# Optimization experiments

Measured on AMD Instinct MI355X. Metric: run time of the kernel, lower is better.

The kernel has to match this reference:

```python
import jax, jax.numpy as jnp
import numpy as np

ALPHA = 0.2  # LeakyReLU negative slope
NEG_INF = -9e15


def setup_inputs() -> dict:
    key = jax.random.key(0)
    k1, k2, k3, k4 = jax.random.split(key, 4)
    B, N, Fin, Fout = 4, 4096, 128, 64
    x = jax.random.normal(k1, (B, N, Fin), dtype=jnp.float32)
    adj = jax.random.randint(k2, (B, N, N), 0, 2, dtype=jnp.int32)
    # xavier_uniform-ish init scale
    W = jax.random.normal(k3, (Fin, Fout), dtype=jnp.float32) * (1.414 / np.sqrt(Fin + Fout))
    a = jax.random.normal(k4, (3 * Fout, 1), dtype=jnp.float32) * (1.414 / np.sqrt(3 * Fout + 1))
    return {"x": x, "adj": adj, "W": W, "a": a}


def reference(x, adj, W, a):
    # h: [B, N, Fout]
    h = jnp.matmul(x, W)
    Fout = W.shape[1]
    # Original builds a_input[b,i,j] = [h_i, h_j, h_i*h_j] and dots with a.
    # Decompose a into the three blocks; identical math, no O(N^2*3F) tensor.
    a1 = a[:Fout, 0]            # weights on h_i (self)
    a2 = a[Fout:2 * Fout, 0]    # weights on h_j (neighbor)
    a3 = a[2 * Fout:, 0]        # weights on h_i * h_j (corr)
    s_self = jnp.einsum('bnf,f->bn', h, a1)        # [B,N]
    s_nei = jnp.einsum('bnf,f->bn', h, a2)         # [B,N]
    s_corr = jnp.einsum('bif,bjf->bij', h * a3, h)  # [B,N,N]
    e = s_self[:, :, None] + s_nei[:, None, :] + s_corr
    e = jnp.where(e > 0, e, ALPHA * e)  # LeakyReLU
    att = jnp.where(adj > 0, e, NEG_INF)
    att = jax.nn.softmax(att, axis=-1)
    # dropout=0.0 / eval mode -> no dropout
    h_prime = jnp.matmul(att, h)  # [B,N,Fout]
    return jax.nn.elu(h_prime)    # concat=True
```

## Files before the change

kernel.cpp:

```cpp
#include <hip/hip_runtime.h>


typedef __attribute__((ext_vector_type(4))) float f32x4;
typedef __attribute__((ext_vector_type(4))) _Float16 h16x4;
typedef __attribute__((ext_vector_type(8))) _Float16 h16x8;
typedef __attribute__((ext_vector_type(2))) __fp16 fp16x2;

#define L2E 1.4426950408889634f

__global__ __launch_bounds__(256) void gat_phase1(
    const float* __restrict__ x,
    const float* __restrict__ W,
    const float* __restrict__ a,
    _Float16* __restrict__ h16,
    _Float16* __restrict__ hT16,
    _Float16* __restrict__ q16,
    float* __restrict__ sS,
    float* __restrict__ sN)
{
  __shared__ float xs[32 * 132];
  __shared__ float ws[128 * 64];
  const int tid = threadIdx.x;
  const int bx  = blockIdx.x;
  const int b   = bx >> 7;
  const int n0  = (bx & 127) << 5;
  const float* xb = x + ((size_t)b * 4096 + n0) * 128;

#pragma unroll
  for (int p = 0; p < 4; ++p) {
    int idx = tid + p * 256;
    int row = idx >> 5, c4 = idx & 31;
    float4 v = ((const float4*)(xb + row * 128))[c4];
    *(float4*)&xs[row * 132 + c4 * 4] = v;
  }
#pragma unroll
  for (int p = 0; p < 8; ++p) {
    int idx = tid + p * 256;
    ((float4*)ws)[idx] = ((const float4*)W)[idx];
  }
  __syncthreads();

  const int tx = tid & 15;
  const int ty = tid >> 4;
  f32x4 acc0 = (f32x4){0.f, 0.f, 0.f, 0.f};
  f32x4 acc1 = (f32x4){0.f, 0.f, 0.f, 0.f};

#pragma unroll 8
  for (int k = 0; k < 128; k += 4) {
    f32x4 x0 = *(const f32x4*)&xs[(2 * ty) * 132 + k];
    f32x4 x1 = *(const f32x4*)&xs[(2 * ty + 1) * 132 + k];
    f32x4 w0 = *(const f32x4*)&ws[(k + 0) * 64 + 4 * tx];
    f32x4 w1 = *(const f32x4*)&ws[(k + 1) * 64 + 4 * tx];
    f32x4 w2 = *(const f32x4*)&ws[(k + 2) * 64 + 4 * tx];
    f32x4 w3 = *(const f32x4*)&ws[(k + 3) * 64 + 4 * tx];
    acc0 += x0.x * w0 + x0.y * w1 + x0.z * w2 + x0.w * w3;
    acc1 += x1.x * w0 + x1.y * w1 + x1.z * w2 + x1.w * w3;
  }
  float acc[2][4] = {{acc0.x, acc0.y, acc0.z, acc0.w},
                     {acc1.x, acc1.y, acc1.z, acc1.w}};

  float a1r[4], a2r[4], a3r[4];
#pragma unroll
  for (int f = 0; f < 4; ++f) {
    a1r[f] = a[4 * tx + f] * L2E;
    a2r[f] = a[64 + 4 * tx + f] * L2E;
    a3r[f] = a[128 + 4 * tx + f] * L2E;
  }
  const size_t bN = (size_t)b * 4096;
#pragma unroll
  for (int r = 0; r < 2; ++r) {
    float p1 = 0.f, p2 = 0.f;
#pragma unroll
    for (int f = 0; f < 4; ++f) { p1 += acc[r][f] * a1r[f]; p2 += acc[r][f] * a2r[f]; }
#pragma unroll
    for (int m = 1; m < 16; m <<= 1) {
      p1 += __shfl_xor(p1, m, 64);
      p2 += __shfl_xor(p2, m, 64);
    }
    if (tx == 0) {
      int n = n0 + 2 * ty + r;
      sS[bN + n] = p1;
      sN[bN + n] = p2;
    }
  }
#pragma unroll
  for (int r = 0; r < 2; ++r) {
    int n = n0 + 2 * ty + r;
    h16x4 hv, qv;
#pragma unroll
    for (int f = 0; f < 4; ++f) {
      hv[f] = (_Float16)acc[r][f];
      qv[f] = (_Float16)(acc[r][f] * a3r[f]);
    }
    *(h16x4*)&h16[(bN + n) * 64 + 4 * tx] = hv;
    *(h16x4*)&q16[(bN + n) * 64 + 4 * tx] = qv;
  }
  __syncthreads();
  _Float16* hTs = (_Float16*)xs;
#pragma unroll
  for (int f = 0; f < 4; ++f)
#pragma unroll
    for (int r = 0; r < 2; ++r)
      hTs[(4 * tx + f) * 40 + 2 * ty + r] = (_Float16)acc[r][f];
  __syncthreads();
  {
    int f = tid >> 2, part = tid & 3;
    uint4 v = *(uint4*)&hTs[f * 40 + 8 * part];
    *(uint4*)&hT16[((size_t)b * 64 + f) * 4096 + n0 + 8 * part] = v;
  }
}

__global__ __launch_bounds__(256, 4) void gat_phase2(
    const _Float16* __restrict__ h16,
    const _Float16* __restrict__ hT16,
    const _Float16* __restrict__ q16,
    const float* __restrict__ sS,
    const float* __restrict__ sN,
    const int* __restrict__ adj,
    float* __restrict__ Opart,
    float* __restrict__ lpart)
{
  __shared__ _Float16 Kb[2][4096];
  __shared__ _Float16 Tb[2][4096];
  __shared__ float sNl[1024];

  const int tid = threadIdx.x;
  const int w = tid >> 6, lane = tid & 63;
  const int qd = lane >> 4, c = lane & 15;
  const int bx = blockIdx.x;
  const int b = bx & 3;
  const int split = (bx >> 2) & 3;
  const int it = bx >> 4;
  const int i0 = it * 64 + w * 16;
  const int jq0 = split * 1024;
  const size_t bN = (size_t)b * 4096;

  const _Float16* qrow = q16 + (bN + i0 + c) * 64;
  h16x8 Qf0 = *(const h16x8*)(qrow + qd * 8);
  h16x8 Qf1 = *(const h16x8*)(qrow + 32 + qd * 8);
  const float ss = sS[bN + i0 + c];

  const int* abase = adj + (bN + i0 + c) * 4096 + jq0 + 4 * qd;

  const int srow = tid >> 3, chunk = tid & 7;
  const int ksw = (chunk ^ (srow & 7)) << 3;
  const int tsw = (chunk ^ ((srow >> 1) & 7)) << 3;
  const bool tswap = (srow & 1);
  const _Float16* hsrc = h16 + (bN + jq0 + srow) * 64 + chunk * 8;
  const _Float16* tsrc = hT16 + ((size_t)b * 64 + srow) * 4096 + jq0 + chunk * 8;

  f32x4 O[4];
#pragma unroll
  for (int ft = 0; ft < 4; ++ft) O[ft] = (f32x4){0.f, 0.f, 0.f, 0.f};
  float lsum = 0.f;

  {
    uint4 k0 = *(const uint4*)hsrc, k1 = *(const uint4*)(hsrc + 32 * 64);
    uint4 t0 = *(const uint4*)tsrc, t1 = *(const uint4*)(tsrc + 32 * 4096);
    *(uint4*)&Kb[0][srow * 64 + ksw] = k0;
    *(uint4*)&Kb[0][(srow + 32) * 64 + ksw] = k1;
    uint4 s0 = tswap ? (uint4){t0.z, t0.w, t0.x, t0.y} : t0;
    uint4 s1 = tswap ? (uint4){t1.z, t1.w, t1.x, t1.y} : t1;
    *(uint4*)&Tb[0][srow * 64 + tsw] = s0;
    *(uint4*)&Tb[0][(srow + 32) * 64 + tsw] = s1;
  }
  ((f32x4*)sNl)[tid] = *(const f32x4*)(sN + bN + jq0 + 4 * tid);
  uint4 av[4];
#pragma unroll
  for (int ct = 0; ct < 4; ++ct) av[ct] = *(const uint4*)(abase + 16 * ct);

  for (int t = 0; t < 16; ++t) {
    __syncthreads();

    uint4 kr0, kr1, tr0, tr1;
    uint4 avn[4] = {av[0], av[1], av[2], av[3]};
    if (t < 15) {
      const _Float16* hs = hsrc + (t + 1) * 4096;
      const _Float16* ts = tsrc + (t + 1) * 64;
      kr0 = *(const uint4*)hs; kr1 = *(const uint4*)(hs + 32 * 64);
      tr0 = *(const uint4*)ts; tr1 = *(const uint4*)(ts + 32 * 4096);
#pragma unroll
      for (int ct = 0; ct < 4; ++ct)
        avn[ct] = *(const uint4*)(abase + (t + 1) * 64 + 16 * ct);
    }

    const _Float16* Kc = &Kb[t & 1][0];
    const _Float16* Tc = &Tb[t & 1][0];
#pragma unroll
    for (int ct = 0; ct < 4; ++ct) {
      const int krow = 16 * ct + c;
      h16x8 Kf0 = *(const h16x8*)&Kc[krow * 64 + ((qd ^ (c & 7)) << 3)];
      h16x8 Kf1 = *(const h16x8*)&Kc[krow * 64 + (((qd + 4) ^ (c & 7)) << 3)];
      f32x4 Sv = (f32x4){0.f, 0.f, 0.f, 0.f};
      Sv = __builtin_amdgcn_mfma_f32_16x16x32_f16(Kf0, Qf0, Sv, 0, 0, 0);
      Sv = __builtin_amdgcn_mfma_f32_16x16x32_f16(Kf1, Qf1, Sv, 0, 0, 0);

      f32x4 snv = ((const f32x4*)sNl)[t * 16 + 4 * ct + qd];
      f32x4 ev = Sv + snv + ss;
      f32x4 tv = __builtin_elementwise_max(ev, ev * 0.2f);
      float p0 = __builtin_amdgcn_exp2f(tv.x);
      float p1 = __builtin_amdgcn_exp2f(tv.y);
      float p2 = __builtin_amdgcn_exp2f(tv.z);
      float p3 = __builtin_amdgcn_exp2f(tv.w);
      p0 = av[ct].x ? p0 : 0.f;
      p1 = av[ct].y ? p1 : 0.f;
      p2 = av[ct].z ? p2 : 0.f;
      p3 = av[ct].w ? p3 : 0.f;
      lsum += (p0 + p1) + (p2 + p3);
      fp16x2 plo = __builtin_amdgcn_cvt_pkrtz(p0, p1);
      fp16x2 phi = __builtin_amdgcn_cvt_pkrtz(p2, p3);
      h16x4 Pf = (h16x4){(_Float16)plo.x, (_Float16)plo.y,
                         (_Float16)phi.x, (_Float16)phi.y};

#pragma unroll
      for (int ft = 0; ft < 4; ++ft) {
        h16x4 Vf = *(const h16x4*)&Tc[(16 * ft + c) * 64 +
                                      (((4 * ct + qd) ^ c) << 2)];
        O[ft] = __builtin_amdgcn_mfma_f32_16x16x16f16(Vf, Pf, O[ft], 0, 0, 0);
      }
    }

    if (t < 15) {
      _Float16* K2 = &Kb[(t & 1) ^ 1][0];
      _Float16* T2 = &Tb[(t & 1) ^ 1][0];
      *(uint4*)&K2[srow * 64 + ksw] = kr0;
      *(uint4*)&K2[(srow + 32) * 64 + ksw] = kr1;
      uint4 s0 = tswap ? (uint4){tr0.z, tr0.w, tr0.x, tr0.y} : tr0;
      uint4 s1 = tswap ? (uint4){tr1.z, tr1.w, tr1.x, tr1.y} : tr1;
      *(uint4*)&T2[srow * 64 + tsw] = s0;
      *(uint4*)&T2[(srow + 32) * 64 + tsw] = s1;
    }
#pragma unroll
    for (int ct = 0; ct < 4; ++ct) av[ct] = avn[ct];
  }

  lsum += __shfl_xor(lsum, 16, 64);
  lsum += __shfl_xor(lsum, 32, 64);

  float* orow = Opart + ((size_t)split * 16384 + bN + i0 + c) * 64;
#pragma unroll
  for (int ft = 0; ft < 4; ++ft)
    *(f32x4*)(orow + 16 * ft + 4 * qd) = O[ft];
  if (lane < 16) lpart[split * 16384 + bN + i0 + c] = lsum;
}

__global__ __launch_bounds__(256) void gat_combine(
    const float* __restrict__ Opart, const float* __restrict__ lpart,
    float* __restrict__ out)
{
  const int tid = threadIdx.x;
  const size_t row = (size_t)blockIdx.x * 16 + (tid >> 4);
  const int f4 = (tid & 15) * 4;
  const size_t R = 16384;
  float l = lpart[row] + lpart[R + row] + lpart[2 * R + row] + lpart[3 * R + row];
  f32x4 o = *(const f32x4*)&Opart[row * 64 + f4];
  o += *(const f32x4*)&Opart[(R + row) * 64 + f4];
  o += *(const f32x4*)&Opart[(2 * R + row) * 64 + f4];
  o += *(const f32x4*)&Opart[(3 * R + row) * 64 + f4];
  float inv = 1.0f / l;
  float4 res;
  float v;
  v = o.x * inv; res.x = v > 0.f ? v : __expf(v) - 1.f;
  v = o.y * inv; res.y = v > 0.f ? v : __expf(v) - 1.f;
  v = o.z * inv; res.z = v > 0.f ? v : __expf(v) - 1.f;
  v = o.w * inv; res.w = v > 0.f ? v : __expf(v) - 1.f;
  *(float4*)&out[row * 64 + f4] = res;
}

extern "C" void kernel_launch(void* const* d_in, const int* in_sizes, int n_in,
                              void* d_out, int out_size, void* d_ws, size_t ws_size,
                              hipStream_t stream) {
  const float* x  = (const float*)d_in[0];
  const int* adj  = (const int*)d_in[1];
  const float* W  = (const float*)d_in[2];
  const float* a  = (const float*)d_in[3];
  float* out = (float*)d_out;

  char* ws = (char*)d_ws;
  _Float16* h16  = (_Float16*)(ws);
  _Float16* hT16 = (_Float16*)(ws + (2u << 20));
  _Float16* q16  = (_Float16*)(ws + (4u << 20));
  float* sS = (float*)(ws + (6u << 20));
  float* sN = (float*)(ws + (6u << 20) + (64u << 10));
  float* Opart = (float*)(ws + (6u << 20) + (128u << 10));
  float* lpart = (float*)(ws + (6u << 20) + (128u << 10) + (17u << 20));

  gat_phase1<<<512, 256, 0, stream>>>(x, W, a, h16, hT16, q16, sS, sN);
  gat_phase2<<<1024, 256, 0, stream>>>(h16, hT16, q16, sS, sN, adj, Opart, lpart);
  gat_combine<<<1024, 256, 0, stream>>>(Opart, lpart, out);
}
```

Measured before the change: 394.5 us.

## Precompute adjacency bitmask in separate kernel and consume bits in attention pass

Adds a pre-pass kernel that streams the int32 adjacency matrix and packs it into 64-bit ballot bitmasks. The attention kernel then reads one 64-bit word per 64 columns instead of sixteen int32 values per lane per tile. This cuts that kernel's memory traffic and register use for adjacency prefetch, so its loop can be bound by compute rather than memory. In exchange there is an extra launch and a full pass over adjacency with narrow 4-byte loads, so the large read is moved rather than removed.

```diff
diff --git a/kernel.cpp b/kernel.cpp
--- a/kernel.cpp
+++ b/kernel.cpp
@@ -7,6 +7,23 @@
 typedef __attribute__((ext_vector_type(2))) __fp16 fp16x2;
 
 #define L2E 1.4426950408889634f
+
+__global__ __launch_bounds__(256) void gat_mask(
+    const int* __restrict__ adj,
+    unsigned long long* __restrict__ mask)
+{
+  const int tid = threadIdx.x;
+  const int w = tid >> 6, lane = tid & 63;
+  const size_t row = (size_t)blockIdx.x * 4 + w;
+  const int* ap = adj + row * 4096 + lane;
+  unsigned long long* mp = mask + row * 64;
+#pragma unroll 4
+  for (int s = 0; s < 64; ++s) {
+    int v = ap[s * 64];
+    unsigned long long m = __ballot(v > 0);
+    if (lane == 0) mp[s] = m;
+  }
+}
 
 __global__ __launch_bounds__(256) void gat_phase1(
     const float* __restrict__ x,
@@ -116,7 +133,7 @@
     const _Float16* __restrict__ q16,
     const float* __restrict__ sS,
     const float* __restrict__ sN,
-    const int* __restrict__ adj,
+    const unsigned long long* __restrict__ mask,
     float* __restrict__ Opart,
     float* __restrict__ lpart)
 {
@@ -140,7 +157,7 @@
   h16x8 Qf1 = *(const h16x8*)(qrow + 32 + qd * 8);
   const float ss = sS[bN + i0 + c];
 
-  const int* abase = adj + (bN + i0 + c) * 4096 + jq0 + 4 * qd;
+  const unsigned long long* mrow = mask + (bN + i0 + c) * 64 + (jq0 >> 6);
 
   const int srow = tid >> 3, chunk = tid & 7;
   const int ksw = (chunk ^ (srow & 7)) << 3;
@@ -165,23 +182,19 @@
     *(uint4*)&Tb[0][(srow + 32) * 64 + tsw] = s1;
   }
   ((f32x4*)sNl)[tid] = *(const f32x4*)(sN + bN + jq0 + 4 * tid);
-  uint4 av[4];
-#pragma unroll
-  for (int ct = 0; ct < 4; ++ct) av[ct] = *(const uint4*)(abase + 16 * ct);
+  unsigned long long m64 = mrow[0];
 
   for (int t = 0; t < 16; ++t) {
     __syncthreads();
 
     uint4 kr0, kr1, tr0, tr1;
-    uint4 avn[4] = {av[0], av[1], av[2], av[3]};
+    unsigned long long mn = m64;
     if (t < 15) {
       const _Float16* hs = hsrc + (t + 1) * 4096;
       const _Float16* ts = tsrc + (t + 1) * 64;
       kr0 = *(const uint4*)hs; kr1 = *(const uint4*)(hs + 32 * 64);
       tr0 = *(const uint4*)ts; tr1 = *(const uint4*)(ts + 32 * 4096);
-#pragma unroll
-      for (int ct = 0; ct < 4; ++ct)
-        avn[ct] = *(const uint4*)(abase + (t + 1) * 64 + 16 * ct);
+      mn = mrow[t + 1];
     }
 
     const _Float16* Kc = &Kb[t & 1][0];
@@ -198,14 +211,15 @@
       f32x4 snv = ((const f32x4*)sNl)[t * 16 + 4 * ct + qd];
       f32x4 ev = Sv + snv + ss;
       f32x4 tv = __builtin_elementwise_max(ev, ev * 0.2f);
+      unsigned bits = (unsigned)(m64 >> (16 * ct + 4 * qd));
       float p0 = __builtin_amdgcn_exp2f(tv.x);
       float p1 = __builtin_amdgcn_exp2f(tv.y);
       float p2 = __builtin_amdgcn_exp2f(tv.z);
       float p3 = __builtin_amdgcn_exp2f(tv.w);
-      p0 = av[ct].x ? p0 : 0.f;
-      p1 = av[ct].y ? p1 : 0.f;
-      p2 = av[ct].z ? p2 : 0.f;
-      p3 = av[ct].w ? p3 : 0.f;
+      p0 = (bits & 1u) ? p0 : 0.f;
+      p1 = (bits & 2u) ? p1 : 0.f;
+      p2 = (bits & 4u) ? p2 : 0.f;
+      p3 = (bits & 8u) ? p3 : 0.f;
       lsum += (p0 + p1) + (p2 + p3);
       fp16x2 plo = __builtin_amdgcn_cvt_pkrtz(p0, p1);
       fp16x2 phi = __builtin_amdgcn_cvt_pkrtz(p2, p3);
@@ -230,8 +244,7 @@
       *(uint4*)&T2[srow * 64 + tsw] = s0;
       *(uint4*)&T2[(srow + 32) * 64 + tsw] = s1;
     }
-#pragma unroll
-    for (int ct = 0; ct < 4; ++ct) av[ct] = avn[ct];
+    m64 = mn;
   }
 
   lsum += __shfl_xor(lsum, 16, 64);
@@ -284,8 +297,11 @@
   float* sN = (float*)(ws + (6u << 20) + (64u << 10));
   float* Opart = (float*)(ws + (6u << 20) + (128u << 10));
   float* lpart = (float*)(ws + (6u << 20) + (128u << 10) + (17u << 20));
-
+  unsigned long long* mask =
+      (unsigned long long*)(ws + (6u << 20) + (128u << 10) + (18u << 20));
+
+  gat_mask<<<4096, 256, 0, stream>>>(adj, mask);
   gat_phase1<<<512, 256, 0, stream>>>(x, W, a, h16, hT16, q16, sS, sN);
-  gat_phase2<<<1024, 256, 0, stream>>>(h16, hT16, q16, sS, sN, adj, Opart, lpart);
+  gat_phase2<<<1024, 256, 0, stream>>>(h16, hT16, q16, sS, sN, mask, Opart, lpart);
   gat_combine<<<1024, 256, 0, stream>>>(Opart, lpart, out);
 }
```

Result: slower. 440.0 us (+11.5%).

## Precompute adjacency bitmask in separate kernel and consume bits in attention loop

Applied to the files above, without the earlier changes.

Adds a kernel that converts the int32 adjacency matrix into a 64-bit-per-word bitmask using wave ballots. The main attention kernel then loads 8-byte mask words instead of streaming 16-byte int vectors per step. This cuts adjacency traffic and register pressure inside the compute loop, at the cost of an extra launch and a separate full pass over adj.

```diff
diff --git a/kernel.cpp b/kernel.cpp
--- a/kernel.cpp
+++ b/kernel.cpp
@@ -5,8 +5,35 @@
 typedef __attribute__((ext_vector_type(4))) _Float16 h16x4;
 typedef __attribute__((ext_vector_type(8))) _Float16 h16x8;
 typedef __attribute__((ext_vector_type(2))) __fp16 fp16x2;
+typedef unsigned long long u64;
 
 #define L2E 1.4426950408889634f
+
+__global__ __launch_bounds__(256) void gat_mask(
+    const int* __restrict__ adj,
+    u64* __restrict__ mask)
+{
+  const int tid = threadIdx.x;
+  const int w = tid >> 6, lane = tid & 63;
+  const size_t row = blockIdx.x;
+  const int* ap = adj + row * 4096;
+  u64* mp = mask + row * 64;
+#pragma unroll
+  for (int p = 0; p < 4; ++p) {
+    const int k = w + 4 * p;
+    int4 v = *(const int4*)(ap + k * 256 + 4 * lane);
+    u64 b0 = __ballot(v.x > 0);
+    u64 b1 = __ballot(v.y > 0);
+    u64 b2 = __ballot(v.z > 0);
+    u64 b3 = __ballot(v.w > 0);
+    if (lane == 0) {
+      mp[4 * k + 0] = b0;
+      mp[4 * k + 1] = b1;
+      mp[4 * k + 2] = b2;
+      mp[4 * k + 3] = b3;
+    }
+  }
+}
 
 __global__ __launch_bounds__(256) void gat_phase1(
     const float* __restrict__ x,
@@ -116,7 +143,7 @@
     const _Float16* __restrict__ q16,
     const float* __restrict__ sS,
     const float* __restrict__ sN,
-    const int* __restrict__ adj,
+    const u64* __restrict__ mask,
     float* __restrict__ Opart,
     float* __restrict__ lpart)
 {
@@ -140,7 +167,7 @@
   h16x8 Qf1 = *(const h16x8*)(qrow + 32 + qd * 8);
   const float ss = sS[bN + i0 + c];
 
-  const int* abase = adj + (bN + i0 + c) * 4096 + jq0 + 4 * qd;
+  const u64* mrow = mask + (bN + i0 + c) * 64 + (jq0 >> 8) * 4;
 
   const int srow = tid >> 3, chunk = tid & 7;
   const int ksw = (chunk ^ (srow & 7)) << 3;
@@ -165,73 +192,80 @@
     *(uint4*)&Tb[0][(srow + 32) * 64 + tsw] = s1;
   }
   ((f32x4*)sNl)[tid] = *(const f32x4*)(sN + bN + jq0 + 4 * tid);
-  uint4 av[4];
-#pragma unroll
-  for (int ct = 0; ct < 4; ++ct) av[ct] = *(const uint4*)(abase + 16 * ct);
-
-  for (int t = 0; t < 16; ++t) {
-    __syncthreads();
-
-    uint4 kr0, kr1, tr0, tr1;
-    uint4 avn[4] = {av[0], av[1], av[2], av[3]};
-    if (t < 15) {
-      const _Float16* hs = hsrc + (t + 1) * 4096;
-      const _Float16* ts = tsrc + (t + 1) * 64;
-      kr0 = *(const uint4*)hs; kr1 = *(const uint4*)(hs + 32 * 64);
-      tr0 = *(const uint4*)ts; tr1 = *(const uint4*)(ts + 32 * 4096);
-#pragma unroll
-      for (int ct = 0; ct < 4; ++ct)
-        avn[ct] = *(const uint4*)(abase + (t + 1) * 64 + 16 * ct);
-    }
-
-    const _Float16* Kc = &Kb[t & 1][0];
-    const _Float16* Tc = &Tb[t & 1][0];
-#pragma unroll
-    for (int ct = 0; ct < 4; ++ct) {
-      const int krow = 16 * ct + c;
-      h16x8 Kf0 = *(const h16x8*)&Kc[krow * 64 + ((qd ^ (c & 7)) << 3)];
-      h16x8 Kf1 = *(const h16x8*)&Kc[krow * 64 + (((qd + 4) ^ (c & 7)) << 3)];
-      f32x4 Sv = (f32x4){0.f, 0.f, 0.f, 0.f};
-      Sv = __builtin_amdgcn_mfma_f32_16x16x32_f16(Kf0, Qf0, Sv, 0, 0, 0);
-      Sv = __builtin_amdgcn_mfma_f32_16x16x32_f16(Kf1, Qf1, Sv, 0, 0, 0);
-
-      f32x4 snv = ((const f32x4*)sNl)[t * 16 + 4 * ct + qd];
-      f32x4 ev = Sv + snv + ss;
-      f32x4 tv = __builtin_elementwise_max(ev, ev * 0.2f);
-      float p0 = __builtin_amdgcn_exp2f(tv.x);
-      float p1 = __builtin_amdgcn_exp2f(tv.y);
-      float p2 = __builtin_amdgcn_exp2f(tv.z);
-      float p3 = __builtin_amdgcn_exp2f(tv.w);
-      p0 = av[ct].x ? p0 : 0.f;
-      p1 = av[ct].y ? p1 : 0.f;
-      p2 = av[ct].z ? p2 : 0.f;
-      p3 = av[ct].w ? p3 : 0.f;
-      lsum += (p0 + p1) + (p2 + p3);
-      fp16x2 plo = __builtin_amdgcn_cvt_pkrtz(p0, p1);
-      fp16x2 phi = __builtin_amdgcn_cvt_pkrtz(p2, p3);
-      h16x4 Pf = (h16x4){(_Float16)plo.x, (_Float16)plo.y,
-                         (_Float16)phi.x, (_Float16)phi.y};
-
-#pragma unroll
-      for (int ft = 0; ft < 4; ++ft) {
-        h16x4 Vf = *(const h16x4*)&Tc[(16 * ft + c) * 64 +
-                                      (((4 * ct + qd) ^ c) << 2)];
-        O[ft] = __builtin_amdgcn_mfma_f32_16x16x16f16(Vf, Pf, O[ft], 0, 0, 0);
+  u64 W0 = mrow[0], W1 = mrow[1], W2 = mrow[2], W3 = mrow[3];
+
+  for (int g = 0; g < 4; ++g) {
+    u64 N0 = W0, N1 = W1, N2 = W2, N3 = W3;
+    if (g < 3) {
+      const u64* mg = mrow + 4 * (g + 1);
+      N0 = mg[0]; N1 = mg[1]; N2 = mg[2]; N3 = mg[3];
+    }
+#pragma unroll
+    for (int tt = 0; tt < 4; ++tt) {
+      const int t = 4 * g + tt;
+      __syncthreads();
+
+      uint4 kr0, kr1, tr0, tr1;
+      if (t < 15) {
+        const _Float16* hs = hsrc + (t + 1) * 4096;
+        const _Float16* ts = tsrc + (t + 1) * 64;
+        kr0 = *(const uint4*)hs; kr1 = *(const uint4*)(hs + 32 * 64);
+        tr0 = *(const uint4*)ts; tr1 = *(const uint4*)(ts + 32 * 4096);
       }
-    }
-
-    if (t < 15) {
-      _Float16* K2 = &Kb[(t & 1) ^ 1][0];
-      _Float16* T2 = &Tb[(t & 1) ^ 1][0];
-      *(uint4*)&K2[srow * 64 + ksw] = kr0;
-      *(uint4*)&K2[(srow + 32) * 64 + ksw] = kr1;
-      uint4 s0 = tswap ? (uint4){tr0.z, tr0.w, tr0.x, tr0.y} : tr0;
-      uint4 s1 = tswap ? (uint4){tr1.z, tr1.w, tr1.x, tr1.y} : tr1;
-      *(uint4*)&T2[srow * 64 + tsw] = s0;
-      *(uint4*)&T2[(srow + 32) * 64 + tsw] = s1;
-    }
-#pragma unroll
-    for (int ct = 0; ct < 4; ++ct) av[ct] = avn[ct];
+
+      const unsigned T0 = ((unsigned)(W0 >> (16 * tt))) >> qd;
+      const unsigned T1 = ((unsigned)(W1 >> (16 * tt))) >> qd;
+      const unsigned T2 = ((unsigned)(W2 >> (16 * tt))) >> qd;
+      const unsigned T3 = ((unsigned)(W3 >> (16 * tt))) >> qd;
+
+      const _Float16* Kc = &Kb[t & 1][0];
+      const _Float16* Tc = &Tb[t & 1][0];
+#pragma unroll
+      for (int ct = 0; ct < 4; ++ct) {
+        const int krow = 16 * ct + c;
+        h16x8 Kf0 = *(const h16x8*)&Kc[krow * 64 + ((qd ^ (c & 7)) << 3)];
+        h16x8 Kf1 = *(const h16x8*)&Kc[krow * 64 + (((qd + 4) ^ (c & 7)) << 3)];
+        f32x4 Sv = (f32x4){0.f, 0.f, 0.f, 0.f};
+        Sv = __builtin_amdgcn_mfma_f32_16x16x32_f16(Kf0, Qf0, Sv, 0, 0, 0);
+        Sv = __builtin_amdgcn_mfma_f32_16x16x32_f16(Kf1, Qf1, Sv, 0, 0, 0);
+
+        f32x4 snv = ((const f32x4*)sNl)[t * 16 + 4 * ct + qd];
+        f32x4 ev = Sv + snv + ss;
+        f32x4 tv = __builtin_elementwise_max(ev, ev * 0.2f);
+        float p0 = __builtin_amdgcn_exp2f(tv.x);
+        float p1 = __builtin_amdgcn_exp2f(tv.y);
+        float p2 = __builtin_amdgcn_exp2f(tv.z);
+        float p3 = __builtin_amdgcn_exp2f(tv.w);
+        p0 = ((T0 >> (4 * ct)) & 1u) ? p0 : 0.f;
+        p1 = ((T1 >> (4 * ct)) & 1u) ? p1 : 0.f;
+        p2 = ((T2 >> (4 * ct)) & 1u) ? p2 : 0.f;
+        p3 = ((T3 >> (4 * ct)) & 1u) ? p3 : 0.f;
+        lsum += (p0 + p1) + (p2 + p3);
+        fp16x2 plo = __builtin_amdgcn_cvt_pkrtz(p0, p1);
+        fp16x2 phi = __builtin_amdgcn_cvt_pkrtz(p2, p3);
+        h16x4 Pf = (h16x4){(_Float16)plo.x, (_Float16)plo.y,
+                           (_Float16)phi.x, (_Float16)phi.y};
+
+#pragma unroll
+        for (int ft = 0; ft < 4; ++ft) {
+          h16x4 Vf = *(const h16x4*)&Tc[(16 * ft + c) * 64 +
+                                        (((4 * ct + qd) ^ c) << 2)];
+          O[ft] = __builtin_amdgcn_mfma_f32_16x16x16f16(Vf, Pf, O[ft], 0, 0, 0);
+        }
+      }
+
+      if (t < 15) {
+        _Float16* K2 = &Kb[(t & 1) ^ 1][0];
+        _Float16* T2 = &Tb[(t & 1) ^ 1][0];
+        *(uint4*)&K2[srow * 64 + ksw] = kr0;
+        *(uint4*)&K2[(srow + 32) * 64 + ksw] = kr1;
+        uint4 s0 = tswap ? (uint4){tr0.z, tr0.w, tr0.x, tr0.y} : tr0;
+        uint4 s1 = tswap ? (uint4){tr1.z, tr1.w, tr1.x, tr1.y} : tr1;
+        *(uint4*)&T2[srow * 64 + tsw] = s0;
+        *(uint4*)&T2[(srow + 32) * 64 + tsw] = s1;
+      }
+    }
+    W0 = N0; W1 = N1; W2 = N2; W3 = N3;
   }
 
   lsum += __shfl_xor(lsum, 16, 64);
@@ -284,8 +318,11 @@
   float* sN = (float*)(ws + (6u << 20) + (64u << 10));
   float* Opart = (float*)(ws + (6u << 20) + (128u << 10));
   float* lpart = (float*)(ws + (6u << 20) + (128u << 10) + (17u << 20));
-
+  u64* mask =
+      (u64*)(ws + (6u << 20) + (128u << 10) + (18u << 20));
+
+  gat_mask<<<16384, 256, 0, stream>>>(adj, mask);
   gat_phase1<<<512, 256, 0, stream>>>(x, W, a, h16, hT16, q16, sS, sN);
-  gat_phase2<<<1024, 256, 0, stream>>>(h16, hT16, q16, sS, sN, adj, Opart, lpart);
+  gat_phase2<<<1024, 256, 0, stream>>>(h16, hT16, q16, sS, sN, mask, Opart, lpart);
   gat_combine<<<1024, 256, 0, stream>>>(Opart, lpart, out);
 }
```

After: 431.5 us. +9.4%, slower.
